# Performance work log

Hardware: AMD Instinct MI355X
Metric: run time of the kernel (lower is better)

## Reference

```python
import jax, jax.numpy as jnp
import numpy as np

# PGA G(3,0,1) blade layout: [1, e0,e1,e2,e3, e01,e02,e03,e12,e13,e23, e012,e013,e023,e123, e0123]
GRADE = jnp.array([0, 1, 1, 1, 1, 2, 2, 2, 2, 2, 2, 3, 3, 3, 3, 4])
# invariant inner product uses only blades not containing the degenerate e0
INNER_IDX = jnp.array([0, 2, 3, 4, 8, 9, 10, 14])

B, N, IN_MV, IN_S = 1, 1024, 16, 128
H, HID_MV, HID_S = 8, 4, 32
C_Z, OUT_MV, OUT_S = 128, 16, 128
ROPE_BASE = 4096.0


def equi_linear(mv, w5):
    # grade-wise equivariant channel mixing: w5 [out, in, 5] -> per-blade weight [out, in, 16]
    w16 = w5[:, :, GRADE]
    return jnp.einsum('...ib,oib->...ob', mv, w16)


def rope(x, base=ROPE_BASE):
    # rotary positional encoding along item axis 1; last dim must be even
    n, d = x.shape[1], x.shape[-1]
    half = d // 2
    freqs = base ** (-jnp.arange(half, dtype=x.dtype) / half)
    ang = jnp.arange(n, dtype=x.dtype)[:, None] * freqs  # [N, half]
    shp = (1, n) + (1,) * (x.ndim - 3) + (half,)
    cos, sin = jnp.cos(ang).reshape(shp), jnp.sin(ang).reshape(shp)
    x1, x2 = x[..., 0::2], x[..., 1::2]
    return jnp.stack([x1 * cos - x2 * sin, x1 * sin + x2 * cos], axis=-1).reshape(x.shape)


def setup_inputs() -> dict:
    key = jax.random.key(0)
    ks = jax.random.split(key, 16)
    sc_mv = 1.0 / np.sqrt(IN_MV)
    sc_s = 1.0 / np.sqrt(IN_S)
    return {
        'mv': jax.random.normal(ks[0], (B, N, IN_MV, 16), jnp.float32),
        's': jax.random.normal(ks[1], (B, N, IN_S), jnp.float32),
        'z': jax.random.normal(ks[2], (B, N, N, C_Z), jnp.float32),
        'q_w_mv': jax.random.normal(ks[3], (H * HID_MV, IN_MV, 5), jnp.float32) * sc_mv,
        'q_w_s': jax.random.normal(ks[4], (H * HID_S, IN_S), jnp.float32) * sc_s,
        'k_w_mv': jax.random.normal(ks[5], (HID_MV, IN_MV, 5), jnp.float32) * sc_mv,
        'k_w_s': jax.random.normal(ks[6], (HID_S, IN_S), jnp.float32) * sc_s,
        'v_w_mv': jax.random.normal(ks[7], (HID_MV, IN_MV, 5), jnp.float32) * sc_mv,
        'v_w_s': jax.random.normal(ks[8], (HID_S, IN_S), jnp.float32) * sc_s,
        'out_w_mv': jax.random.normal(ks[9], (OUT_MV, H * HID_MV, 5), jnp.float32) / np.sqrt(H * HID_MV),
        'out_w_s': jax.random.normal(ks[10], (OUT_S, H * HID_S), jnp.float32) / np.sqrt(H * HID_S),
        'ln_g': jnp.ones((C_Z,), jnp.float32),
        'ln_b': jnp.zeros((C_Z,), jnp.float32),
        'bias_w': jax.random.normal(ks[11], (C_Z, H), jnp.float32) / np.sqrt(C_Z),
    }


def reference(mv, s, z, q_w_mv, q_w_s, k_w_mv, k_w_s, v_w_mv, v_w_s,
              out_w_mv, out_w_s, ln_g, ln_b, bias_w):
    b, n = mv.shape[0], mv.shape[1]
    # multi-query QKV: queries per-head, shared single-head K/V
    q_mv = equi_linear(mv, q_w_mv).reshape(b, n, H, HID_MV, 16)
    q_s = jnp.einsum('bns,os->bno', s, q_w_s).reshape(b, n, H, HID_S)
    k_mv = equi_linear(mv, k_w_mv)                     # [B,N,hid_mv,16]
    k_s = jnp.einsum('bns,os->bno', s, k_w_s)          # [B,N,hid_s]
    v_mv = equi_linear(mv, v_w_mv)
    v_s = jnp.einsum('bns,os->bno', s, v_w_s)
    # rotary encoding on scalar queries/keys
    q_s, k_s = rope(q_s), rope(k_s)
    # invariant attention features: non-degenerate mv components + scalars
    qf = jnp.concatenate([q_mv[..., INNER_IDX].reshape(b, n, H, HID_MV * 8), q_s], axis=-1)
    kf = jnp.concatenate([k_mv[..., INNER_IDX].reshape(b, n, HID_MV * 8), k_s], axis=-1)
    d = qf.shape[-1]
    logits = jnp.einsum('bqhd,bkd->bhqk', qf, kf) / jnp.sqrt(jnp.asarray(d, qf.dtype))
    # pair bias: Linear(LayerNorm(z)) -> heads
    mu = jnp.mean(z, axis=-1, keepdims=True)
    var = jnp.var(z, axis=-1, keepdims=True)
    zn = (z - mu) * jax.lax.rsqrt(var + 1e-5) * ln_g + ln_b
    bias = jnp.einsum('bqkc,ch->bhqk', zn, bias_w)
    attn = jax.nn.softmax(logits + bias, axis=-1)      # [B,H,N,N]
    o_mv = jnp.einsum('bhqk,bkcx->bqhcx', attn, v_mv).reshape(b, n, H * HID_MV, 16)
    o_s = jnp.einsum('bhqk,bkc->bqhc', attn, v_s).reshape(b, n, H * HID_S)
    out_mv = equi_linear(o_mv, out_w_mv)               # [B,N,out_mv,16]
    out_s = jnp.einsum('bnc,oc->bno', o_s, out_w_s)    # [B,N,out_s]
    return out_mv, out_s
```

## Files before the change

### kernel.cpp

```cpp
#include <hip/hip_runtime.h>

__device__ __constant__ int GRADE_C[16] = {0,1,1,1,1,2,2,2,2,2,2,3,3,3,3,4};
__device__ __constant__ int INNER_C[8]  = {0,2,3,4,8,9,10,14};

#define OFF_GH    0
#define GWBT_BYTE 4096
#define KFB_BYTE  16384
#define VTB_BYTE  262144
#define QFB_BYTE  524288
#define SB_BYTE   3145728

typedef __attribute__((ext_vector_type(8))) short bf16x8;
typedef __attribute__((ext_vector_type(4))) float f32x4;
typedef __attribute__((ext_vector_type(4))) unsigned int u32x4;

static __device__ __forceinline__ unsigned short f2bf(float f) {
    unsigned int u = __float_as_uint(f);
    u = u + 0x7fffu + ((u >> 16) & 1u);
    return (unsigned short)(u >> 16);
}
static __device__ __forceinline__ unsigned pk2(float lo, float hi) {
    return (unsigned)f2bf(lo) | ((unsigned)f2bf(hi) << 16);
}
static __device__ __forceinline__ float bflo(unsigned int u) {
    return __uint_as_float(u << 16);
}
static __device__ __forceinline__ float bfhi(unsigned int u) {
    return __uint_as_float(u & 0xffff0000u);
}

__global__ __launch_bounds__(256) void kproj(
    const float* __restrict__ mv, const float* __restrict__ s,
    const float* __restrict__ q_w_mv, const float* __restrict__ q_w_s,
    const float* __restrict__ k_w_mv, const float* __restrict__ k_w_s,
    const float* __restrict__ v_w_mv, const float* __restrict__ v_w_s,
    const float* __restrict__ ln_g, const float* __restrict__ ln_b,
    const float* __restrict__ bias_w, float* __restrict__ ws)
{
    __shared__ __align__(16) float mvn[256];
    __shared__ __align__(16) float sn[128];
    __shared__ float qs_pre[256];
    __shared__ float ks_pre[32];
    __shared__ float vs_pre[32];
    const int n = blockIdx.x, t = threadIdx.x;

    unsigned short* kfb = (unsigned short*)((char*)ws + KFB_BYTE);
    unsigned short* qfb = (unsigned short*)((char*)ws + QFB_BYTE);
    unsigned short* gwp = (unsigned short*)((char*)ws + GWBT_BYTE);
    unsigned short* vtb = (unsigned short*)((char*)ws + VTB_BYTE);

    mvn[t] = mv[n * 256 + t];
    if (t < 128) sn[t] = s[n * 128 + t];
    __syncthreads();

    {
        const float4* w = (const float4*)(q_w_s + t * 128);
        const float4* sv = (const float4*)sn;
        float acc = 0.f;
        #pragma unroll
        for (int c4 = 0; c4 < 32; ++c4) {
            float4 wv = w[c4], x = sv[c4];
            acc += wv.x * x.x + wv.y * x.y + wv.z * x.z + wv.w * x.w;
        }
        qs_pre[t] = acc;
    }
    if (t < 64) {
        const float* wb = (t < 32) ? (k_w_s + t * 128) : (v_w_s + (t - 32) * 128);
        const float4* w = (const float4*)wb;
        const float4* sv = (const float4*)sn;
        float acc = 0.f;
        #pragma unroll
        for (int c4 = 0; c4 < 32; ++c4) {
            float4 wv = w[c4], x = sv[c4];
            acc += wv.x * x.x + wv.y * x.y + wv.z * x.z + wv.w * x.w;
        }
        if (t < 32) ks_pre[t] = acc; else vs_pre[t - 32] = acc;
    }
    {
        int o = t >> 3, j = t & 7;
        int bx = INNER_C[j], g = GRADE_C[bx];
        float acc = 0.f;
        #pragma unroll
        for (int i = 0; i < 16; ++i)
            acc += mvn[i * 16 + bx] * q_w_mv[(o * 16 + i) * 5 + g];
        int h = o >> 2, c = o & 3, d = c * 8 + j;
        qfb[n * 1024 + h * 64 + d] = f2bf(acc);
    }
    {
        int hp = 8 + (t >> 5), d = t & 31;
        qfb[n * 1024 + hp * 64 + d] = 0;
        qfb[n * 1024 + hp * 64 + 32 + d] = 0;
    }
    if (t < 32) {
        int bx = INNER_C[t & 7], g = GRADE_C[bx];
        float acc = 0.f;
        #pragma unroll
        for (int i = 0; i < 16; ++i)
            acc += mvn[i * 16 + bx] * k_w_mv[((t >> 3) * 16 + i) * 5 + g];
        kfb[n * 64 + t] = f2bf(acc);
    }
    if (t >= 64 && t < 128) {
        int idx = t - 64, x = idx & 15, g = GRADE_C[x];
        float acc = 0.f;
        #pragma unroll
        for (int i = 0; i < 16; ++i)
            acc += mvn[i * 16 + x] * v_w_mv[((idx >> 4) * 16 + i) * 5 + g];
        vtb[idx * 1024 + n] = f2bf(acc);
    }
    __syncthreads();

    {
        int h = t >> 5, dd = t & 31, i = dd >> 1;
        float freq = exp2f(-0.75f * (float)i);
        float ang = (float)n * freq;
        float cv = cosf(ang), sv = sinf(ang);
        float x1 = qs_pre[h * 32 + 2 * i], x2 = qs_pre[h * 32 + 2 * i + 1];
        float val = ((dd & 1) == 0) ? (x1 * cv - x2 * sv) : (x1 * sv + x2 * cv);
        qfb[n * 1024 + h * 64 + 32 + dd] = f2bf(val);
    }
    if (t < 32) {
        int i = t >> 1;
        float freq = exp2f(-0.75f * (float)i);
        float ang = (float)n * freq;
        float cv = cosf(ang), sv = sinf(ang);
        float x1 = ks_pre[2 * i], x2 = ks_pre[2 * i + 1];
        float val = ((t & 1) == 0) ? (x1 * cv - x2 * sv) : (x1 * sv + x2 * cv);
        kfb[n * 64 + 32 + t] = f2bf(val);
    }
    if (t >= 32 && t < 64) vtb[(64 + t - 32) * 1024 + n] = f2bf(vs_pre[t - 32]);

    if (n == 0) {
        if (t < 128) {
            int cb = t >> 5, r = t & 31;
            int lg, e;
            if (r < 16) { lg = r >> 2; e = r & 3; }
            else        { lg = (r - 16) >> 2; e = 4 + (r & 3); }
            int pos = cb * 32 + lg * 8 + e;
            float g = ln_g[t];
            #pragma unroll
            for (int j = 0; j < 8; ++j)
                gwp[j * 128 + pos] = f2bf(g * bias_w[t * 8 + j]);
            gwp[8 * 128 + pos] = 0x3F80;
            #pragma unroll
            for (int j = 9; j < 16; ++j) gwp[j * 128 + pos] = 0;
        }
        if (t >= 128 && t < 136) {
            int h = t - 128;
            float gh = 0.f, ch = 0.f;
            for (int c = 0; c < 128; ++c) {
                gh += ln_g[c] * bias_w[c * 8 + h];
                ch += ln_b[c] * bias_w[c * 8 + h];
            }
            ws[OFF_GH + h] = gh;
            ws[OFF_GH + 8 + h] = ch;
        }
    }
}

__global__ __launch_bounds__(256, 4) void kbias(
    const float* __restrict__ z, float* __restrict__ ws)
{
    __shared__ float d1[128][17];
    __shared__ float d2[128][17];
    __shared__ float ssq[128];
    const int blk = blockIdx.x;
    const int q = blk >> 3, kblk = blk & 7;
    const int t = threadIdx.x, w = t >> 6, l = t & 63;
    const int lm = l & 15, lg = l >> 4;

    bf16x8 B1[4], B2[2];
    #pragma unroll
    for (int ks = 0; ks < 4; ++ks)
        B1[ks] = *(const bf16x8*)((const char*)ws + GWBT_BYTE + (lm * 128 + ks * 32 + lg * 8) * 2);
    #pragma unroll
    for (int ds = 0; ds < 2; ++ds)
        B2[ds] = *(const bf16x8*)((const char*)ws + QFB_BYTE + ((size_t)q * 1024 + lm * 64 + ds * 32 + lg * 8) * 2);

    #pragma unroll
    for (int mi = 0; mi < 2; ++mi) {
        const int mt = w * 2 + mi;
        const int krow = kblk * 128 + mt * 16 + lm;
        const float* zr = z + ((size_t)q * 1024 + krow) * 128 + lg * 4;
        float4 za[4], zb[4];
        #pragma unroll
        for (int ks = 0; ks < 4; ++ks) {
            za[ks] = *(const float4*)(zr + ks * 32);
            zb[ks] = *(const float4*)(zr + ks * 32 + 16);
        }
        bf16x8 A2[2];
        #pragma unroll
        for (int ds = 0; ds < 2; ++ds)
            A2[ds] = *(const bf16x8*)((const char*)ws + KFB_BYTE + ((size_t)krow * 64 + ds * 32 + lg * 8) * 2);

        f32x4 acc1 = {0.f, 0.f, 0.f, 0.f};
        f32x4 acc2 = {0.f, 0.f, 0.f, 0.f};
        float sq = 0.f;
        #pragma unroll
        for (int ks = 0; ks < 4; ++ks) {
            float xs[8] = {za[ks].x, za[ks].y, za[ks].z, za[ks].w,
                           zb[ks].x, zb[ks].y, zb[ks].z, zb[ks].w};
            #pragma unroll
            for (int e = 0; e < 8; ++e) sq = __builtin_fmaf(xs[e], xs[e], sq);
            u32x4 au;
            au[0] = pk2(xs[0], xs[1]); au[1] = pk2(xs[2], xs[3]);
            au[2] = pk2(xs[4], xs[5]); au[3] = pk2(xs[6], xs[7]);
            bf16x8 af = __builtin_bit_cast(bf16x8, au);
            acc1 = __builtin_amdgcn_mfma_f32_16x16x32_bf16(af, B1[ks], acc1, 0, 0, 0);
        }
        acc2 = __builtin_amdgcn_mfma_f32_16x16x32_bf16(A2[0], B2[0], acc2, 0, 0, 0);
        acc2 = __builtin_amdgcn_mfma_f32_16x16x32_bf16(A2[1], B2[1], acc2, 0, 0, 0);

        sq += __shfl_xor(sq, 16);
        sq += __shfl_xor(sq, 32);
        if (lg == 0) ssq[mt * 16 + lm] = sq;

        #pragma unroll
        for (int r = 0; r < 4; ++r) {
            int row = mt * 16 + lg * 4 + r;
            d1[row][lm] = acc1[r];
            d2[row][lm] = acc2[r];
        }
    }
    __syncthreads();

    {
        const int r = t >> 1, hb = t & 1;
        float sum = d1[r][8];
        float sq = ssq[r];
        float mean = sum * (1.f / 128.f);
        float var = sq * (1.f / 128.f) - mean * mean;
        float rs = rsqrtf(var + 1e-5f);
        unsigned short u[4];
        #pragma unroll
        for (int j = 0; j < 4; ++j) {
            int h = hb * 4 + j;
            float bias = rs * (d1[r][h] - mean * ws[OFF_GH + h]) + ws[OFF_GH + 8 + h];
            u[j] = f2bf(d2[r][h] * 0.125f + bias);
        }
        uint2 pk;
        pk.x = (unsigned)u[0] | ((unsigned)u[1] << 16);
        pk.y = (unsigned)u[2] | ((unsigned)u[3] << 16);
        unsigned short* sb = (unsigned short*)((char*)ws + SB_BYTE);
        *(uint2*)(sb + ((size_t)q * 1024 + kblk * 128 + r) * 8 + hb * 4) = pk;
    }
}

__global__ __launch_bounds__(256) void kattn(
    const float* __restrict__ ws,
    const float* __restrict__ out_w_mv, const float* __restrict__ out_w_s,
    float* __restrict__ d_out)
{
    __shared__ __align__(16) unsigned int Pb[16 * 512];
    __shared__ float inv_l[8];
    __shared__ float o_sh[8 * 96];
    const int q = blockIdx.x, t = threadIdx.x;

    const unsigned short* sb =
        (const unsigned short*)((const char*)ws + SB_BYTE) + (size_t)q * 8192;
    #pragma unroll
    for (int it = 0; it < 2; ++it) {
        int wd = it * 256 + t;
        uint4 r0 = *(const uint4*)(sb + (size_t)wd * 16);
        uint4 r1 = *(const uint4*)(sb + (size_t)wd * 16 + 8);
        Pb[0 * 512 + (wd ^ (0 << 2))] = (r0.x & 0xffffu) | (r1.x << 16);
        Pb[1 * 512 + (wd ^ (1 << 2))] = (r0.x >> 16) | (r1.x & 0xffff0000u);
        Pb[2 * 512 + (wd ^ (2 << 2))] = (r0.y & 0xffffu) | (r1.y << 16);
        Pb[3 * 512 + (wd ^ (3 << 2))] = (r0.y >> 16) | (r1.y & 0xffff0000u);
        Pb[4 * 512 + (wd ^ (4 << 2))] = (r0.z & 0xffffu) | (r1.z << 16);
        Pb[5 * 512 + (wd ^ (5 << 2))] = (r0.z >> 16) | (r1.z & 0xffff0000u);
        Pb[6 * 512 + (wd ^ (6 << 2))] = (r0.w & 0xffffu) | (r1.w << 16);
        Pb[7 * 512 + (wd ^ (7 << 2))] = (r0.w >> 16) | (r1.w & 0xffff0000u);
    }
    __syncthreads();

    const int h = t >> 5, e = t & 31;
    const int hx = (h & 7) << 2;
    unsigned int* Ph = &Pb[h * 512];
    float m = -1e30f;
    #pragma unroll
    for (int j = 0; j < 16; ++j) {
        unsigned int v = Ph[(e + j * 32) ^ hx];
        m = fmaxf(m, fmaxf(bflo(v), bfhi(v)));
    }
    #pragma unroll
    for (int d = 16; d >= 1; d >>= 1) m = fmaxf(m, __shfl_xor(m, d));
    float lsum = 0.f;
    #pragma unroll
    for (int j = 0; j < 16; ++j) {
        int idx = (e + j * 32) ^ hx;
        unsigned int v = Ph[idx];
        float p0 = __expf(bflo(v) - m);
        float p1 = __expf(bfhi(v) - m);
        lsum += p0 + p1;
        Ph[idx] = pk2(p0, p1);
    }
    #pragma unroll
    for (int d = 16; d >= 1; d >>= 1) lsum += __shfl_xor(lsum, d);
    if (e == 0) inv_l[h] = 1.f / lsum;
    __syncthreads();

    const int wv = t >> 6, l = t & 63, lm = l & 15, lg = l >> 4;
    const unsigned short* vtb = (const unsigned short*)((const char*)ws + VTB_BYTE);
    const char* PbB = (const char*)Pb;
    const int nmt = (wv < 2) ? 2 : 1;
    for (int ii = 0; ii < nmt; ++ii) {
        int mt = wv + ii * 4;
        f32x4 acc = {0.f, 0.f, 0.f, 0.f};
        #pragma unroll 8
        for (int ks = 0; ks < 32; ++ks) {
            bf16x8 a = *(const bf16x8*)(vtb + (size_t)(mt * 16 + lm) * 1024 + ks * 32 + lg * 8);
            bf16x8 b = *(const bf16x8*)(PbB + lm * 2048 + ((ks * 64 + lg * 16) ^ ((lm & 7) << 4)));
            acc = __builtin_amdgcn_mfma_f32_16x16x32_bf16(a, b, acc, 0, 0, 0);
        }
        if (lm < 8) {
            float il = inv_l[lm];
            #pragma unroll
            for (int r = 0; r < 4; ++r)
                o_sh[lm * 96 + mt * 16 + lg * 4 + r] = acc[r] * il;
        }
    }
    __syncthreads();

    {
        int o2 = t >> 4, b = t & 15, g = GRADE_C[b];
        float acc = 0.f;
        #pragma unroll
        for (int i = 0; i < 32; ++i)
            acc += o_sh[(i >> 2) * 96 + (i & 3) * 16 + b] *
                   out_w_mv[(o2 * 32 + i) * 5 + g];
        d_out[(q * 16 + o2) * 16 + b] = acc;
    }
    if (t < 128) {
        const float* wv2 = out_w_s + t * 256;
        float acc = 0.f;
        #pragma unroll 4
        for (int c = 0; c < 256; ++c)
            acc += o_sh[(c >> 5) * 96 + 64 + (c & 31)] * wv2[c];
        d_out[262144 + q * 128 + t] = acc;
    }
}

extern "C" void kernel_launch(void* const* d_in, const int* in_sizes, int n_in,
                              void* d_out, int out_size, void* d_ws, size_t ws_size,
                              hipStream_t stream) {
    (void)in_sizes; (void)n_in; (void)out_size; (void)ws_size;
    const float* mv       = (const float*)d_in[0];
    const float* s        = (const float*)d_in[1];
    const float* z        = (const float*)d_in[2];
    const float* q_w_mv   = (const float*)d_in[3];
    const float* q_w_s    = (const float*)d_in[4];
    const float* k_w_mv   = (const float*)d_in[5];
    const float* k_w_s    = (const float*)d_in[6];
    const float* v_w_mv   = (const float*)d_in[7];
    const float* v_w_s    = (const float*)d_in[8];
    const float* out_w_mv = (const float*)d_in[9];
    const float* out_w_s  = (const float*)d_in[10];
    const float* ln_g     = (const float*)d_in[11];
    const float* ln_b     = (const float*)d_in[12];
    const float* bias_w   = (const float*)d_in[13];
    float* ws  = (float*)d_ws;
    float* out = (float*)d_out;

    kproj<<<1024, 256, 0, stream>>>(mv, s, q_w_mv, q_w_s, k_w_mv, k_w_s,
                                    v_w_mv, v_w_s, ln_g, ln_b, bias_w, ws);
    kbias<<<8192, 256, 0, stream>>>(z, ws);
    kattn<<<1024, 256, 0, stream>>>(ws, out_w_mv, out_w_s, out);
}
```

Measured before the change: 194.2 us.

## Hoist z loads, use hardware bf16 pack, widen attention blocks to 512 threads

The bias kernel now issues all z loads for both M-tiles up front, so more memory requests are in flight before the MFMA work starts. It also swaps the manual round-to-nearest bf16 conversion for the packed HIP bf16 conversion intrinsic. The attention kernel runs 512 threads per block: one wave per head does the softmax and six waves each take one MFMA tile, with the output projections split across disjoint thread ranges. The trade-offs are higher register pressure in the bias kernel and fewer co-resident blocks per CU for the larger attention blocks.

```diff
diff --git a/kernel.cpp b/kernel.cpp
--- a/kernel.cpp
+++ b/kernel.cpp
@@ -1,4 +1,5 @@
 #include <hip/hip_runtime.h>
+#include <hip/hip_bf16.h>
 
 __device__ __constant__ int GRADE_C[16] = {0,1,1,1,1,2,2,2,2,2,2,3,3,3,3,4};
 __device__ __constant__ int INNER_C[8]  = {0,2,3,4,8,9,10,14};
@@ -21,6 +22,12 @@
 }
 static __device__ __forceinline__ unsigned pk2(float lo, float hi) {
     return (unsigned)f2bf(lo) | ((unsigned)f2bf(hi) << 16);
+}
+static __device__ __forceinline__ unsigned cvtpk(float lo, float hi) {
+    __hip_bfloat162 c = __float22bfloat162_rn(make_float2(lo, hi));
+    unsigned u;
+    __builtin_memcpy(&u, &c, 4);
+    return u;
 }
 static __device__ __forceinline__ float bflo(unsigned int u) {
     return __uint_as_float(u << 16);
@@ -176,17 +183,22 @@
     for (int ds = 0; ds < 2; ++ds)
         B2[ds] = *(const bf16x8*)((const char*)ws + QFB_BYTE + ((size_t)q * 1024 + lm * 64 + ds * 32 + lg * 8) * 2);
 
+    float4 za[2][4], zb[2][4];
+    #pragma unroll
+    for (int mi = 0; mi < 2; ++mi) {
+        const int krow = kblk * 128 + (w * 2 + mi) * 16 + lm;
+        const float* zr = z + ((size_t)q * 1024 + krow) * 128 + lg * 4;
+        #pragma unroll
+        for (int ks = 0; ks < 4; ++ks) {
+            za[mi][ks] = *(const float4*)(zr + ks * 32);
+            zb[mi][ks] = *(const float4*)(zr + ks * 32 + 16);
+        }
+    }
+
     #pragma unroll
     for (int mi = 0; mi < 2; ++mi) {
         const int mt = w * 2 + mi;
         const int krow = kblk * 128 + mt * 16 + lm;
-        const float* zr = z + ((size_t)q * 1024 + krow) * 128 + lg * 4;
-        float4 za[4], zb[4];
-        #pragma unroll
-        for (int ks = 0; ks < 4; ++ks) {
-            za[ks] = *(const float4*)(zr + ks * 32);
-            zb[ks] = *(const float4*)(zr + ks * 32 + 16);
-        }
         bf16x8 A2[2];
         #pragma unroll
         for (int ds = 0; ds < 2; ++ds)
@@ -197,13 +209,14 @@
         float sq = 0.f;
         #pragma unroll
         for (int ks = 0; ks < 4; ++ks) {
-            float xs[8] = {za[ks].x, za[ks].y, za[ks].z, za[ks].w,
-                           zb[ks].x, zb[ks].y, zb[ks].z, zb[ks].w};
-            #pragma unroll
-            for (int e = 0; e < 8; ++e) sq = __builtin_fmaf(xs[e], xs[e], sq);
+            float4 A = za[mi][ks], Bv = zb[mi][ks];
+            sq = __builtin_fmaf(A.x, A.x, sq);  sq = __builtin_fmaf(A.y, A.y, sq);
+            sq = __builtin_fmaf(A.z, A.z, sq);  sq = __builtin_fmaf(A.w, A.w, sq);
+            sq = __builtin_fmaf(Bv.x, Bv.x, sq); sq = __builtin_fmaf(Bv.y, Bv.y, sq);
+            sq = __builtin_fmaf(Bv.z, Bv.z, sq); sq = __builtin_fmaf(Bv.w, Bv.w, sq);
             u32x4 au;
-            au[0] = pk2(xs[0], xs[1]); au[1] = pk2(xs[2], xs[3]);
-            au[2] = pk2(xs[4], xs[5]); au[3] = pk2(xs[6], xs[7]);
+            au[0] = cvtpk(A.x, A.y);   au[1] = cvtpk(A.z, A.w);
+            au[2] = cvtpk(Bv.x, Bv.y); au[3] = cvtpk(Bv.z, Bv.w);
             bf16x8 af = __builtin_bit_cast(bf16x8, au);
             acc1 = __builtin_amdgcn_mfma_f32_16x16x32_bf16(af, B1[ks], acc1, 0, 0, 0);
         }
@@ -245,7 +258,7 @@
     }
 }
 
-__global__ __launch_bounds__(256) void kattn(
+__global__ __launch_bounds__(512) void kattn(
     const float* __restrict__ ws,
     const float* __restrict__ out_w_mv, const float* __restrict__ out_w_s,
     float* __restrict__ d_out)
@@ -257,9 +270,8 @@
 
     const unsigned short* sb =
         (const unsigned short*)((const char*)ws + SB_BYTE) + (size_t)q * 8192;
-    #pragma unroll
-    for (int it = 0; it < 2; ++it) {
-        int wd = it * 256 + t;
+    {
+        int wd = t;
         uint4 r0 = *(const uint4*)(sb + (size_t)wd * 16);
         uint4 r1 = *(const uint4*)(sb + (size_t)wd * 16 + 8);
         Pb[0 * 512 + (wd ^ (0 << 2))] = (r0.x & 0xffffu) | (r1.x << 16);
@@ -273,21 +285,21 @@
     }
     __syncthreads();
 
-    const int h = t >> 5, e = t & 31;
+    const int h = t >> 6, e = t & 63;
     const int hx = (h & 7) << 2;
     unsigned int* Ph = &Pb[h * 512];
     float m = -1e30f;
     #pragma unroll
-    for (int j = 0; j < 16; ++j) {
-        unsigned int v = Ph[(e + j * 32) ^ hx];
+    for (int j = 0; j < 8; ++j) {
+        unsigned int v = Ph[(e + j * 64) ^ hx];
         m = fmaxf(m, fmaxf(bflo(v), bfhi(v)));
     }
     #pragma unroll
-    for (int d = 16; d >= 1; d >>= 1) m = fmaxf(m, __shfl_xor(m, d));
+    for (int d = 32; d >= 1; d >>= 1) m = fmaxf(m, __shfl_xor(m, d));
     float lsum = 0.f;
     #pragma unroll
-    for (int j = 0; j < 16; ++j) {
-        int idx = (e + j * 32) ^ hx;
+    for (int j = 0; j < 8; ++j) {
+        int idx = (e + j * 64) ^ hx;
         unsigned int v = Ph[idx];
         float p0 = __expf(bflo(v) - m);
         float p1 = __expf(bfhi(v) - m);
@@ -295,16 +307,15 @@
         Ph[idx] = pk2(p0, p1);
     }
     #pragma unroll
-    for (int d = 16; d >= 1; d >>= 1) lsum += __shfl_xor(lsum, d);
+    for (int d = 32; d >= 1; d >>= 1) lsum += __shfl_xor(lsum, d);
     if (e == 0) inv_l[h] = 1.f / lsum;
     __syncthreads();
 
     const int wv = t >> 6, l = t & 63, lm = l & 15, lg = l >> 4;
     const unsigned short* vtb = (const unsigned short*)((const char*)ws + VTB_BYTE);
     const char* PbB = (const char*)Pb;
-    const int nmt = (wv < 2) ? 2 : 1;
-    for (int ii = 0; ii < nmt; ++ii) {
-        int mt = wv + ii * 4;
+    if (wv < 6) {
+        int mt = wv;
         f32x4 acc = {0.f, 0.f, 0.f, 0.f};
         #pragma unroll 8
         for (int ks = 0; ks < 32; ++ks) {
@@ -321,7 +332,7 @@
     }
     __syncthreads();
 
-    {
+    if (t < 256) {
         int o2 = t >> 4, b = t & 15, g = GRADE_C[b];
         float acc = 0.f;
         #pragma unroll
@@ -330,13 +341,14 @@
                    out_w_mv[(o2 * 32 + i) * 5 + g];
         d_out[(q * 16 + o2) * 16 + b] = acc;
     }
-    if (t < 128) {
-        const float* wv2 = out_w_s + t * 256;
+    if (t >= 256 && t < 384) {
+        int tt = t - 256;
+        const float* wv2 = out_w_s + tt * 256;
         float acc = 0.f;
         #pragma unroll 4
         for (int c = 0; c < 256; ++c)
             acc += o_sh[(c >> 5) * 96 + 64 + (c & 31)] * wv2[c];
-        d_out[262144 + q * 128 + t] = acc;
+        d_out[262144 + q * 128 + tt] = acc;
     }
 }
 
@@ -364,5 +376,5 @@
     kproj<<<1024, 256, 0, stream>>>(mv, s, q_w_mv, q_w_s, k_w_mv, k_w_s,
                                     v_w_mv, v_w_s, ln_g, ln_b, bias_w, ws);
     kbias<<<8192, 256, 0, stream>>>(z, ws);
-    kattn<<<1024, 256, 0, stream>>>(ws, out_w_mv, out_w_s, out);
-}
+    kattn<<<1024, 512, 0, stream>>>(ws, out_w_mv, out_w_s, out);
+}
```

Result: faster. 186.9 us (-3.8%).
